# Kernel tuning notes

Hardware: AMD Instinct MI355X
Metric: run time of the kernel (lower is better)

## Reference

```python
import jax, jax.numpy as jnp
import numpy as np


def setup_inputs() -> dict:
    key = jax.random.key(0)
    k1, k2, k3, k4 = jax.random.split(key, 4)
    B, N, D, K, O = 8, 6144, 16, 3, 64
    inputs = jax.random.normal(k1, (B, N, D), dtype=jnp.float32)
    supports = jax.random.uniform(k2, (K, N, N), dtype=jnp.float32)
    W = jax.random.normal(k3, (O, D * K), dtype=jnp.float32) * 0.05
    b = jax.random.normal(k4, (O,), dtype=jnp.float32) * 0.05
    return {"inputs": inputs, "supports": supports, "W": W, "b": b}


def reference(inputs, supports, W, b):
    # inputs: [B, N, D]; supports: [K, N, N]; W: [O, D*K]; b: [O]
    B, N, D = inputs.shape
    K = supports.shape[0]
    # matrix_normalization: support + I  (identity self-loop add)
    sup = supports + jnp.eye(N, dtype=supports.dtype)  # [K, N, N]
    # per-support dense matmul; layout [B, N, D, K] matches the torch
    # stack/reshape/transpose chain (feature index = d*K + k)
    y = jnp.einsum('knm,bmd->bndk', sup, inputs)  # [B, N, D, K]
    y = y.reshape(B, N, D * K)
    return y @ W.T + b  # [B, N, O]
```

## Files before the change

kernel.cpp:

```cpp
#include <hip/hip_runtime.h>

#define NN 6144
#define BND (NN*16)

typedef short short8 __attribute__((ext_vector_type(8)));
typedef float f32x4 __attribute__((ext_vector_type(4)));

__device__ __forceinline__ short f2bf(float f) {
    unsigned u = __builtin_bit_cast(unsigned, f);
    u = (u + 0x7FFFu + ((u >> 16) & 1u)) >> 16;
    return (short)u;
}

__global__ void __launch_bounds__(256) prep_kernel(
    const float* __restrict__ xin, unsigned short* __restrict__ Xt)
{
    __shared__ unsigned short ldsT[16 * 64];
    const int b  = blockIdx.y;
    const int m0 = blockIdx.x * 64;
    const int t  = threadIdx.x;
    const int ml = t >> 2, dq = t & 3;
    float4 v = *(const float4*)(xin + (size_t)b * BND + (size_t)(m0 + ml) * 16 + dq * 4);
    ldsT[(dq * 4 + 0) * 64 + ml] = (unsigned short)f2bf(v.x);
    ldsT[(dq * 4 + 1) * 64 + ml] = (unsigned short)f2bf(v.y);
    ldsT[(dq * 4 + 2) * 64 + ml] = (unsigned short)f2bf(v.z);
    ldsT[(dq * 4 + 3) * 64 + ml] = (unsigned short)f2bf(v.w);
    __syncthreads();
    if (t < 128) {
        int d = t >> 3, j = t & 7;
        short8 s = *(const short8*)&ldsT[d * 64 + j * 8];
        *(short8*)(Xt + (size_t)(b * 16 + d) * NN + m0 + j * 8) = s;
    }
}

__global__ void __launch_bounds__(256, 4) gemm_kernel(
    const float* __restrict__ sup, const float* __restrict__ xin,
    const unsigned short* __restrict__ Xt, float* __restrict__ Yws)
{
    __shared__ float lred[4 * 2048];
    const int tid = threadIdx.x;
    const int w = tid >> 6, L = tid & 63, q = L >> 4, col = L & 15;
    const int n0 = blockIdx.x * 16;
    const int k  = blockIdx.y;
    const float* arow = sup + (size_t)k * NN * NN + (size_t)(n0 + col) * NN;
    const unsigned short* xcol = Xt + (size_t)col * NN;

    f32x4 acc[8];
#pragma unroll
    for (int i = 0; i < 8; ++i) acc[i] = (f32x4)0.0f;

    int m0 = w * 1536 + q * 8;
    for (int it = 0; it < 48; ++it, m0 += 32) {
        float4 a0 = *(const float4*)(arow + m0);
        float4 a1 = *(const float4*)(arow + m0 + 4);
        short8 bfr[8];
#pragma unroll
        for (int cc = 0; cc < 8; ++cc)
            bfr[cc] = *(const short8*)(xcol + (size_t)cc * 16 * NN + m0);
        short8 af;
        af[0] = f2bf(a0.x); af[1] = f2bf(a0.y); af[2] = f2bf(a0.z); af[3] = f2bf(a0.w);
        af[4] = f2bf(a1.x); af[5] = f2bf(a1.y); af[6] = f2bf(a1.z); af[7] = f2bf(a1.w);
#pragma unroll
        for (int cc = 0; cc < 8; ++cc)
            acc[cc] = __builtin_amdgcn_mfma_f32_16x16x32_bf16(af, bfr[cc], acc[cc], 0, 0, 0);
    }

#pragma unroll
    for (int cc = 0; cc < 8; ++cc)
#pragma unroll
        for (int r = 0; r < 4; ++r)
            lred[w * 2048 + (q * 4 + r) * 128 + cc * 16 + col] = acc[cc][r];
    __syncthreads();

#pragma unroll
    for (int half = 0; half < 2; ++half) {
        int e = half * 1024 + tid * 4;
        float4 s0 = *(const float4*)&lred[e];
        float4 s1 = *(const float4*)&lred[2048 + e];
        float4 s2 = *(const float4*)&lred[4096 + e];
        float4 s3 = *(const float4*)&lred[6144 + e];
        int r = e >> 7, c = e & 127;
        int n = n0 + r, b = c >> 4, d = c & 15;
        float4 xi = *(const float4*)(xin + (size_t)b * BND + (size_t)n * 16 + d);
        float4 o;
        o.x = s0.x + s1.x + s2.x + s3.x + xi.x;
        o.y = s0.y + s1.y + s2.y + s3.y + xi.y;
        o.z = s0.z + s1.z + s2.z + s3.z + xi.z;
        o.w = s0.w + s1.w + s2.w + s3.w + xi.w;
        *(float4*)(Yws + ((size_t)k * NN + n) * 128 + c) = o;
    }
}

__global__ void __launch_bounds__(256) out_kernel(
    const float* __restrict__ Yws, const float* __restrict__ W,
    const float* __restrict__ bias, float* __restrict__ out)
{
    const int o   = threadIdx.x & 63;
    const int wid = blockIdx.x * 4 + (threadIdx.x >> 6);

    float wreg[48];
#pragma unroll
    for (int d = 0; d < 16; ++d)
#pragma unroll
        for (int kk = 0; kk < 3; ++kk)
            wreg[kk * 16 + d] = W[o * 48 + d * 3 + kk];
    const float bv = bias[o];

    for (int ii = 0; ii < 24; ++ii) {
        int p = wid * 24 + ii;
        int b = p / NN;
        int n = p - b * NN;
        const float* yp = Yws + (size_t)n * 128 + b * 16;
        float acc = bv;
#pragma unroll
        for (int kk = 0; kk < 3; ++kk)
#pragma unroll
            for (int d4 = 0; d4 < 4; ++d4) {
                float4 y = *(const float4*)(yp + (size_t)kk * (NN * 128) + d4 * 4);
                int j = kk * 16 + d4 * 4;
                acc += y.x * wreg[j] + y.y * wreg[j + 1] + y.z * wreg[j + 2] + y.w * wreg[j + 3];
            }
        out[(size_t)p * 64 + o] = acc;
    }
}

extern "C" void kernel_launch(void* const* d_in, const int* in_sizes, int n_in,
                              void* d_out, int out_size, void* d_ws, size_t ws_size,
                              hipStream_t stream) {
    const float* xin  = (const float*)d_in[0];
    const float* sup  = (const float*)d_in[1];
    const float* W    = (const float*)d_in[2];
    const float* bias = (const float*)d_in[3];
    float* out = (float*)d_out;

    char* ws = (char*)d_ws;
    unsigned short* Xt = (unsigned short*)ws;
    float* Yws = (float*)(ws + 1572864);

    prep_kernel<<<dim3(96, 8), 256, 0, stream>>>(xin, Xt);
    gemm_kernel<<<dim3(384, 3), 256, 0, stream>>>(sup, xin, Xt, Yws);
    out_kernel<<<512, 256, 0, stream>>>(Yws, W, bias, out);
}
```

Before: 873.2 us.

## Tile GEMM through LDS with async loads, split-K into bf16 partials

The GEMM kernel now processes 64 rows per block and stages swizzled A and X tiles into LDS with global_load_lds, so X columns are shared across four waves instead of each wave re-reading them. K is split into two segments over blockIdx.z, replacing the in-block cross-wave reduction, and partial results are written as bf16 to halve workspace traffic. The identity term is folded into the output kernel through pre-summed weights applied to the raw input. This adds two syncthreads per iteration with no double buffering and adds bf16 rounding of the intermediate partials.

```diff
diff --git a/kernel.cpp b/kernel.cpp
--- a/kernel.cpp
+++ b/kernel.cpp
@@ -10,6 +10,10 @@
     unsigned u = __builtin_bit_cast(unsigned, f);
     u = (u + 0x7FFFu + ((u >> 16) & 1u)) >> 16;
     return (short)u;
+}
+__device__ __forceinline__ float bf2f(unsigned short s) {
+    unsigned u = ((unsigned)s) << 16;
+    return __builtin_bit_cast(float, u);
 }
 
 __global__ void __launch_bounds__(256) prep_kernel(
@@ -34,66 +38,89 @@
 }
 
 __global__ void __launch_bounds__(256, 4) gemm_kernel(
-    const float* __restrict__ sup, const float* __restrict__ xin,
-    const unsigned short* __restrict__ Xt, float* __restrict__ Yws)
+    const float* __restrict__ sup, const unsigned short* __restrict__ Xt,
+    unsigned short* __restrict__ Yp)
 {
-    __shared__ float lred[4 * 2048];
+    __shared__ float ldsram[8192];
+    float* ldsA = ldsram;
+    unsigned short* ldsB = (unsigned short*)(ldsram + 4096);
+
     const int tid = threadIdx.x;
     const int w = tid >> 6, L = tid & 63, q = L >> 4, col = L & 15;
-    const int n0 = blockIdx.x * 16;
-    const int k  = blockIdx.y;
-    const float* arow = sup + (size_t)k * NN * NN + (size_t)(n0 + col) * NN;
-    const unsigned short* xcol = Xt + (size_t)col * NN;
+    const int n0  = blockIdx.x * 64;
+    const int k   = blockIdx.y;
+    const int seg = blockIdx.z;
+    const float* Ab = sup + (size_t)k * NN * NN;
 
     f32x4 acc[8];
 #pragma unroll
     for (int i = 0; i < 8; ++i) acc[i] = (f32x4)0.0f;
 
-    int m0 = w * 1536 + q * 8;
-    for (int it = 0; it < 48; ++it, m0 += 32) {
-        float4 a0 = *(const float4*)(arow + m0);
-        float4 a1 = *(const float4*)(arow + m0 + 4);
-        short8 bfr[8];
+    for (int it = 0; it < 48; ++it) {
+        const int k0 = seg * 3072 + it * 64;
 #pragma unroll
-        for (int cc = 0; cc < 8; ++cc)
-            bfr[cc] = *(const short8*)(xcol + (size_t)cc * 16 * NN + m0);
-        short8 af;
-        af[0] = f2bf(a0.x); af[1] = f2bf(a0.y); af[2] = f2bf(a0.z); af[3] = f2bf(a0.w);
-        af[4] = f2bf(a1.x); af[5] = f2bf(a1.y); af[6] = f2bf(a1.z); af[7] = f2bf(a1.w);
+        for (int i = 0; i < 4; ++i) {
+            int p = i * 256 + tid;
+            int r = p >> 4, cs = p & 15;
+            int cch = cs ^ (r & 7);
+            const float* src = Ab + (size_t)(n0 + r) * NN + k0 + cch * 4;
+            __builtin_amdgcn_global_load_lds(
+                (const __attribute__((address_space(1))) unsigned int*)src,
+                (__attribute__((address_space(3))) unsigned int*)((char*)ldsA + p * 16), 16, 0, 0);
+        }
 #pragma unroll
-        for (int cc = 0; cc < 8; ++cc)
-            acc[cc] = __builtin_amdgcn_mfma_f32_16x16x32_bf16(af, bfr[cc], acc[cc], 0, 0, 0);
+        for (int i = 0; i < 4; ++i) {
+            int p = i * 256 + tid;
+            int c = p >> 3, hs = p & 7;
+            int h = hs ^ (c & 7);
+            const unsigned short* src = Xt + (size_t)c * NN + k0 + h * 8;
+            __builtin_amdgcn_global_load_lds(
+                (const __attribute__((address_space(1))) unsigned int*)src,
+                (__attribute__((address_space(3))) unsigned int*)((char*)ldsB + p * 16), 16, 0, 0);
+        }
+        __syncthreads();
+
+        const int r = w * 16 + col;
+#pragma unroll
+        for (int kc = 0; kc < 2; ++kc) {
+            int c0 = kc * 8 + q * 2;
+            float4 a0 = *(const float4*)&ldsA[(r * 16 + ((c0    ) ^ (r & 7))) * 4];
+            float4 a1 = *(const float4*)&ldsA[(r * 16 + ((c0 + 1) ^ (r & 7))) * 4];
+            short8 af;
+            af[0] = f2bf(a0.x); af[1] = f2bf(a0.y); af[2] = f2bf(a0.z); af[3] = f2bf(a0.w);
+            af[4] = f2bf(a1.x); af[5] = f2bf(a1.y); af[6] = f2bf(a1.z); af[7] = f2bf(a1.w);
+#pragma unroll
+            for (int cc = 0; cc < 8; ++cc) {
+                int c = cc * 16 + col;
+                short8 bf = *(const short8*)&ldsB[(c * 8 + ((kc * 4 + q) ^ (c & 7))) * 8];
+                acc[cc] = __builtin_amdgcn_mfma_f32_16x16x32_bf16(af, bf, acc[cc], 0, 0, 0);
+            }
+        }
+        __syncthreads();
     }
 
+    float* stg = ldsram + w * 2048;
 #pragma unroll
     for (int cc = 0; cc < 8; ++cc)
 #pragma unroll
-        for (int r = 0; r < 4; ++r)
-            lred[w * 2048 + (q * 4 + r) * 128 + cc * 16 + col] = acc[cc][r];
-    __syncthreads();
+        for (int rr = 0; rr < 4; ++rr)
+            stg[(q * 4 + rr) * 128 + cc * 16 + col] = acc[cc][rr];
 
+    unsigned short* ypb = Yp + ((size_t)(seg * 3 + k) * NN + n0 + w * 16) * 128;
 #pragma unroll
-    for (int half = 0; half < 2; ++half) {
-        int e = half * 1024 + tid * 4;
-        float4 s0 = *(const float4*)&lred[e];
-        float4 s1 = *(const float4*)&lred[2048 + e];
-        float4 s2 = *(const float4*)&lred[4096 + e];
-        float4 s3 = *(const float4*)&lred[6144 + e];
-        int r = e >> 7, c = e & 127;
-        int n = n0 + r, b = c >> 4, d = c & 15;
-        float4 xi = *(const float4*)(xin + (size_t)b * BND + (size_t)n * 16 + d);
-        float4 o;
-        o.x = s0.x + s1.x + s2.x + s3.x + xi.x;
-        o.y = s0.y + s1.y + s2.y + s3.y + xi.y;
-        o.z = s0.z + s1.z + s2.z + s3.z + xi.z;
-        o.w = s0.w + s1.w + s2.w + s3.w + xi.w;
-        *(float4*)(Yws + ((size_t)k * NN + n) * 128 + c) = o;
+    for (int u = 0; u < 8; ++u) {
+        int idx = u * 256 + L * 4;
+        float4 v = *(const float4*)&stg[idx];
+        unsigned h0 = (unsigned short)f2bf(v.x) | ((unsigned)(unsigned short)f2bf(v.y) << 16);
+        unsigned h1 = (unsigned short)f2bf(v.z) | ((unsigned)(unsigned short)f2bf(v.w) << 16);
+        uint2 pk; pk.x = h0; pk.y = h1;
+        *(uint2*)(ypb + idx) = pk;
     }
 }
 
 __global__ void __launch_bounds__(256) out_kernel(
-    const float* __restrict__ Yws, const float* __restrict__ W,
-    const float* __restrict__ bias, float* __restrict__ out)
+    const unsigned short* __restrict__ Yp, const float* __restrict__ xin,
+    const float* __restrict__ W, const float* __restrict__ bias, float* __restrict__ out)
 {
     const int o   = threadIdx.x & 63;
     const int wid = blockIdx.x * 4 + (threadIdx.x >> 6);
@@ -104,21 +131,35 @@
 #pragma unroll
         for (int kk = 0; kk < 3; ++kk)
             wreg[kk * 16 + d] = W[o * 48 + d * 3 + kk];
+    float wsum[16];
+#pragma unroll
+    for (int d = 0; d < 16; ++d) wsum[d] = wreg[d] + wreg[16 + d] + wreg[32 + d];
     const float bv = bias[o];
 
     for (int ii = 0; ii < 24; ++ii) {
         int p = wid * 24 + ii;
         int b = p / NN;
         int n = p - b * NN;
-        const float* yp = Yws + (size_t)n * 128 + b * 16;
         float acc = bv;
+        const float* xp = xin + (size_t)b * BND + (size_t)n * 16;
 #pragma unroll
-        for (int kk = 0; kk < 3; ++kk)
+        for (int d4 = 0; d4 < 4; ++d4) {
+            float4 x4 = *(const float4*)(xp + d4 * 4);
+            acc += x4.x * wsum[d4 * 4] + x4.y * wsum[d4 * 4 + 1]
+                 + x4.z * wsum[d4 * 4 + 2] + x4.w * wsum[d4 * 4 + 3];
+        }
 #pragma unroll
-            for (int d4 = 0; d4 < 4; ++d4) {
-                float4 y = *(const float4*)(yp + (size_t)kk * (NN * 128) + d4 * 4);
-                int j = kk * 16 + d4 * 4;
-                acc += y.x * wreg[j] + y.y * wreg[j + 1] + y.z * wreg[j + 2] + y.w * wreg[j + 3];
+        for (int s = 0; s < 2; ++s)
+#pragma unroll
+            for (int kk = 0; kk < 3; ++kk) {
+                const unsigned short* yp = Yp + ((size_t)(s * 3 + kk) * NN + n) * 128 + b * 16;
+                short8 y0 = *(const short8*)yp;
+                short8 y1 = *(const short8*)(yp + 8);
+#pragma unroll
+                for (int j = 0; j < 8; ++j) {
+                    acc += bf2f((unsigned short)y0[j]) * wreg[kk * 16 + j];
+                    acc += bf2f((unsigned short)y1[j]) * wreg[kk * 16 + 8 + j];
+                }
             }
         out[(size_t)p * 64 + o] = acc;
     }
@@ -135,9 +176,9 @@
 
     char* ws = (char*)d_ws;
     unsigned short* Xt = (unsigned short*)ws;
-    float* Yws = (float*)(ws + 1572864);
+    unsigned short* Yp = (unsigned short*)(ws + 1572864);
 
     prep_kernel<<<dim3(96, 8), 256, 0, stream>>>(xin, Xt);
-    gemm_kernel<<<dim3(384, 3), 256, 0, stream>>>(sup, xin, Xt, Yws);
-    out_kernel<<<512, 256, 0, stream>>>(Yws, W, bias, out);
+    gemm_kernel<<<dim3(96, 3, 2), 256, 0, stream>>>(sup, Xt, Yp);
+    out_kernel<<<512, 256, 0, stream>>>(Yp, xin, W, bias, out);
 }
```

Measured after the change: 709.3 us. 18.8% less time.
